# Optimization experiments

Hardware: AMD Instinct MI355X
Metric: run time of the kernel (lower is better)

## Reference

```python
import jax, jax.numpy as jnp
import numpy as np

B, NG, EG = 128, 256, 2048      # graphs, nodes/graph, edges/graph
N, E = B * NG, B * EG
D_NODE, D_EDGE, HID, HEADS = 64, 32, 128, 2
F1 = HEADS * HID                # 256
K = NG // 2                     # SAGPooling ratio=0.5 -> 128 nodes kept/graph


def _glorot(k, shape):
    fan_in = shape[0]
    return jax.random.normal(k, shape, jnp.float32) / np.sqrt(fan_in)


def setup_inputs() -> dict:
    key = jax.random.key(0)
    ks = jax.random.split(key, 26)
    x = jax.random.normal(ks[0], (N, D_NODE), jnp.float32)
    off = (jnp.arange(B, dtype=jnp.int32) * NG)[:, None]
    src = (jax.random.randint(ks[1], (B, EG), 0, NG, jnp.int32) + off).reshape(-1)
    dst = (jax.random.randint(ks[2], (B, EG), 0, NG, jnp.int32) + off).reshape(-1)
    edge_index = jnp.stack([src, dst])
    edge_attr = jax.random.normal(ks[3], (E, D_EDGE), jnp.float32)
    batch = jnp.repeat(jnp.arange(B, dtype=jnp.int32), NG)
    p = {
        'Wl1': _glorot(ks[4], (D_NODE, F1)), 'bl1': jnp.zeros((F1,), jnp.float32),
        'Wr1': _glorot(ks[5], (D_NODE, F1)), 'br1': jnp.zeros((F1,), jnp.float32),
        'We1': _glorot(ks[6], (D_EDGE, F1)),
        'att1': _glorot(ks[7], (HEADS, HID)), 'bout1': jnp.zeros((F1,), jnp.float32),
        'Wl2': _glorot(ks[8], (F1, F1)), 'bl2': jnp.zeros((F1,), jnp.float32),
        'Wr2': _glorot(ks[9], (F1, F1)), 'br2': jnp.zeros((F1,), jnp.float32),
        'We2': _glorot(ks[10], (D_EDGE, F1)),
        'att2': _glorot(ks[11], (1, F1)), 'bout2': jnp.zeros((F1,), jnp.float32),
        'Wrel': _glorot(ks[12], (F1, 1)), 'brel': jnp.zeros((1,), jnp.float32),
        'Wroot': _glorot(ks[13], (F1, 1)),
        'Wlin': _glorot(ks[14], (F1, 1)), 'blin': jnp.zeros((1,), jnp.float32),
    }
    return dict(x=x, edge_index=edge_index, edge_attr=edge_attr, batch=batch, **p)


def _gatv2(x, src, dst, eattr, Wl, bl, Wr, br, We, att, bout, heads, ch):
    n = x.shape[0]
    xl = (x @ Wl + bl).reshape(n, heads, ch)          # source transform (lin_l)
    xr = (x @ Wr + br).reshape(n, heads, ch)          # target transform (lin_r)
    ef = (eattr @ We).reshape(-1, heads, ch)
    m = xl[src] + xr[dst] + ef                        # [Etot, H, C]
    logits = jnp.einsum('ehc,hc->eh', jax.nn.leaky_relu(m, 0.2), att)
    mx = jax.lax.stop_gradient(jax.ops.segment_max(logits, dst, num_segments=n))
    ex = jnp.exp(logits - mx[dst])
    den = jax.ops.segment_sum(ex, dst, num_segments=n)
    alpha = ex / den[dst]                             # segment softmax per target
    out = jax.ops.segment_sum(alpha[:, :, None] * xl[src], dst, num_segments=n)
    return out.reshape(n, heads * ch) + bout


def reference(x, edge_index, edge_attr, batch,
              Wl1, bl1, Wr1, br1, We1, att1, bout1,
              Wl2, bl2, Wr2, br2, We2, att2, bout2,
              Wrel, brel, Wroot, Wlin, blin):
    n = x.shape[0]
    src, dst = edge_index[0], edge_index[1]
    # add_self_loops with fill_value='mean' of incoming edge attrs (PyG default)
    ones = jnp.ones((src.shape[0],), x.dtype)
    cnt = jax.ops.segment_sum(ones, dst, num_segments=n)
    loop_attr = jax.ops.segment_sum(edge_attr, dst, num_segments=n) / jnp.maximum(cnt, 1.0)[:, None]
    ar = jnp.arange(n, dtype=src.dtype)
    srcA = jnp.concatenate([src, ar])
    dstA = jnp.concatenate([dst, ar])
    eA = jnp.concatenate([edge_attr, loop_attr])
    # conv1: GATv2(64 -> 128, heads=2, concat)
    h = _gatv2(x, srcA, dstA, eA, Wl1, bl1, Wr1, br1, We1, att1, bout1, HEADS, HID)
    h = jax.nn.relu(h)
    # conv2: GATv2(256 -> 256, heads=1)
    h = _gatv2(h, srcA, dstA, eA, Wl2, bl2, Wr2, br2, We2, att2, bout2, 1, F1)
    # SAGPooling: GraphConv(256->1) scorer on original edges, tanh, top-k ratio=0.5
    agg = jax.ops.segment_sum(h[src], dst, num_segments=n)
    score = jnp.tanh((agg @ Wrel + brel + h @ Wroot).reshape(-1))
    sv, si = jax.lax.top_k(score.reshape(B, NG), K)   # equal-size graphs -> static k
    hg = h.reshape(B, NG, F1)
    xk = jnp.take_along_axis(hg, si[:, :, None], axis=1) * sv[:, :, None]
    xk = xk.reshape(B * K, F1)
    # dropout is identity in inference mode; final head
    return jax.nn.sigmoid(xk @ Wlin + blin)
```

## Files before the change

kernel.cpp:

```cpp
#include <hip/hip_runtime.h>
#include <math.h>

#define NNODES   32768
#define NEDGES   262144
#define EATOT    (NEDGES + NNODES)
#define NB       128
#define NGR      256
#define KKEEP    128
#define F1DIM    256
#define DNODE    64
#define DEDGE    32

__device__ __forceinline__ float xla_tanhf(float x) {
    float ax = fabsf(x);
    if (ax < 0.0004f) return x;
    if (ax > 7.90531110763549805f) return copysignf(1.0f, x);
    float x2 = __fmul_rn(x, x);
    float p = -2.76076847742355e-16f;
    p = fmaf(p, x2, 2.00018790482477e-13f);
    p = fmaf(p, x2, -8.60467152213735e-11f);
    p = fmaf(p, x2, 5.12229709037114e-08f);
    p = fmaf(p, x2, 1.48572235717979e-05f);
    p = fmaf(p, x2, 6.37261928875436e-04f);
    p = fmaf(p, x2, 4.89352455891786e-03f);
    p = __fmul_rn(x, p);
    float q = 1.19825839466702e-06f;
    q = fmaf(q, x2, 1.18534705686654e-04f);
    q = fmaf(q, x2, 2.26843463243900e-03f);
    q = fmaf(q, x2, 4.89352518554385e-03f);
    return __fdiv_rn(p, q);
}

__global__ void count_kernel(const int* __restrict__ ei, int* __restrict__ deg) {
    int t = blockIdx.x * 256 + threadIdx.x;
    if (t < NEDGES) atomicAdd(&deg[ei[NEDGES + t]], 1);
}

__global__ void scan_kernel(const int* __restrict__ deg, int* __restrict__ rowstart,
                            int* __restrict__ fill) {
    __shared__ int sh[1024];
    int t = threadIdx.x;
    int base = t * 32;
    int local[32];
    int s = 0;
#pragma unroll
    for (int i = 0; i < 32; i++) { local[i] = deg[base + i]; s += local[i]; }
    sh[t] = s;
    __syncthreads();
    for (int off = 1; off < 1024; off <<= 1) {
        int v = 0;
        if (t >= off) v = sh[t - off];
        __syncthreads();
        if (t >= off) sh[t] += v;
        __syncthreads();
    }
    int run = sh[t] - s;
#pragma unroll
    for (int i = 0; i < 32; i++) {
        rowstart[base + i] = run;
        fill[base + i] = run;
        run += local[i];
    }
    if (t == 1023) rowstart[NNODES] = run;
}

__global__ void scatter_kernel(const int* __restrict__ ei, int* __restrict__ fill,
                               int* __restrict__ csr) {
    int t = blockIdx.x * 256 + threadIdx.x;
    if (t < NEDGES) {
        int d = ei[NEDGES + t];
        int slot = atomicAdd(&fill[d], 1);
        csr[slot] = t;
    }
}

__global__ void sortcsr_kernel(const int* __restrict__ rowstart, int* __restrict__ csr) {
    int n = blockIdx.x * 256 + threadIdx.x;
    if (n >= NNODES) return;
    int s0 = rowstart[n], s1 = rowstart[n + 1];
    for (int i = s0 + 1; i < s1; i++) {
        int v = csr[i];
        int j = i - 1;
        while (j >= s0 && csr[j] > v) { csr[j + 1] = csr[j]; j--; }
        csr[j + 1] = v;
    }
}

__global__ void loopattr_kernel(const int* __restrict__ rowstart, const int* __restrict__ csr,
                                const float* __restrict__ eattr, float* __restrict__ loop_attr) {
    int t = blockIdx.x * 256 + threadIdx.x;
    int n = t >> 5, c = t & 31;
    int s0 = rowstart[n], s1 = rowstart[n + 1];
    float sum = 0.f;
    for (int i = s0; i < s1; i++) sum = __fadd_rn(sum, eattr[(size_t)csr[i] * DEDGE + c]);
    float cnt = (float)(s1 - s0);
    loop_attr[t] = __fdiv_rn(sum, fmaxf(cnt, 1.f));
}

template<int KD>
__global__ __launch_bounds__(256) void gemm_lr_kernel(
    const float* __restrict__ X,
    const float* __restrict__ Wl, const float* __restrict__ bl,
    const float* __restrict__ Wr, const float* __restrict__ br,
    float* __restrict__ outL, float* __restrict__ outR) {
    constexpr int NPB = 16;
    int n0 = __builtin_amdgcn_readfirstlane(blockIdx.x) * NPB;
    const float* __restrict__ Xb = X + (size_t)n0 * KD;
    int c = threadIdx.x;
    float accL[NPB], accR[NPB];
#pragma unroll
    for (int m = 0; m < NPB; m++) { accL[m] = 0.f; accR[m] = 0.f; }
    for (int k = 0; k < KD; k++) {
        float wl = Wl[k * F1DIM + c];
        float wr = Wr[k * F1DIM + c];
#pragma unroll
        for (int m = 0; m < NPB; m++) {
            float xv = Xb[m * KD + k];
            accL[m] = fmaf(xv, wl, accL[m]);
            accR[m] = fmaf(xv, wr, accR[m]);
        }
    }
    float blc = bl[c], brc = br[c];
#pragma unroll
    for (int m = 0; m < NPB; m++) {
        outL[(size_t)(n0 + m) * F1DIM + c] = __fadd_rn(accL[m], blc);
        outR[(size_t)(n0 + m) * F1DIM + c] = __fadd_rn(accR[m], brc);
    }
}

template<int H>
__global__ __launch_bounds__(256) void logits_kernel(
    const int* __restrict__ ei,
    const float* __restrict__ eattr, const float* __restrict__ loop_attr,
    const float* __restrict__ xl, const float* __restrict__ xr,
    const float* __restrict__ We, const float* __restrict__ att,
    float* __restrict__ logits) {
    constexpr int TILE = 8;
    constexpr int EPAD = 260;
    __shared__ float stageF[4][TILE * EPAD];
    int t = threadIdx.x;
    int lane = t & 63;
    int wv = t >> 6;

    float4 wreg[DEDGE];
#pragma unroll
    for (int k = 0; k < DEDGE; k++) wreg[k] = ((const float4*)We)[k * 64 + lane];
    float4 a4 = ((const float4*)att)[lane];

    int wid = (blockIdx.x * 256 + t) >> 6;
    int nw = (gridDim.x * 256) >> 6;
    int ntiles = EATOT / TILE;

    for (int tile = wid; tile < ntiles; tile += nw) {
        int ebase = __builtin_amdgcn_readfirstlane(tile) * TILE;

        for (int ee = 0; ee < TILE; ee++) {
            int e = ebase + ee;
            int s, d;
            const float* ea;
            if (e < NEDGES) {
                s = ei[e]; d = ei[NEDGES + e];
                ea = eattr + (size_t)e * DEDGE;
            } else {
                s = e - NEDGES; d = s;
                ea = loop_attr + (size_t)(e - NEDGES) * DEDGE;
            }
            s = __builtin_amdgcn_readfirstlane(s);
            d = __builtin_amdgcn_readfirstlane(d);
            float ef0 = 0.f, ef1 = 0.f, ef2 = 0.f, ef3 = 0.f;
#pragma unroll
            for (int k = 0; k < DEDGE; k++) {
                float eak = ea[k];
                ef0 = fmaf(eak, wreg[k].x, ef0);
                ef1 = fmaf(eak, wreg[k].y, ef1);
                ef2 = fmaf(eak, wreg[k].z, ef2);
                ef3 = fmaf(eak, wreg[k].w, ef3);
            }
            float4 l4 = ((const float4*)(xl + (size_t)s * F1DIM))[lane];
            float4 r4 = ((const float4*)(xr + (size_t)d * F1DIM))[lane];
            float mv, lk;
            float4 pv;
            mv = __fadd_rn(__fadd_rn(l4.x, r4.x), ef0);
            lk = mv > 0.f ? mv : __fmul_rn(0.2f, mv);
            pv.x = __fmul_rn(lk, a4.x);
            mv = __fadd_rn(__fadd_rn(l4.y, r4.y), ef1);
            lk = mv > 0.f ? mv : __fmul_rn(0.2f, mv);
            pv.y = __fmul_rn(lk, a4.y);
            mv = __fadd_rn(__fadd_rn(l4.z, r4.z), ef2);
            lk = mv > 0.f ? mv : __fmul_rn(0.2f, mv);
            pv.z = __fmul_rn(lk, a4.z);
            mv = __fadd_rn(__fadd_rn(l4.w, r4.w), ef3);
            lk = mv > 0.f ? mv : __fmul_rn(0.2f, mv);
            pv.w = __fmul_rn(lk, a4.w);
            *(float4*)&stageF[wv][ee * EPAD + lane * 4] = pv;
        }

        if (H == 2) {
            int edge = lane >> 3;
            int half = (lane >> 2) & 1;
            int j = lane & 3;
            const float* base = &stageF[wv][edge * EPAD + half * 128 + j];
            float s = 0.f;
#pragma unroll
            for (int L = 0; L < 32; L++)
                s = __fadd_rn(s, base[L * 4]);
            float o = __fadd_rn(s, __shfl_xor(s, 2));
            float r = __fadd_rn(o, __shfl_xor(o, 1));
            if (j == 0) logits[(size_t)(ebase + edge) * 2 + half] = r;
        } else {
            float s = 0.f;
            if (lane < 32) {
                int edge = lane >> 2;
                int j = lane & 3;
                const float* base = &stageF[wv][edge * EPAD + j];
#pragma unroll
                for (int L = 0; L < 64; L++)
                    s = __fadd_rn(s, base[L * 4]);
                float o = __fadd_rn(s, __shfl_xor(s, 2));
                float r = __fadd_rn(o, __shfl_xor(o, 1));
                if ((lane & 3) == 0) logits[ebase + (lane >> 2)] = r;
            }
        }
    }
}

template<int H>
__global__ void softmax_kernel(const int* __restrict__ rowstart, const int* __restrict__ csr,
                               const float* __restrict__ logits, float* __restrict__ w) {
    int t = blockIdx.x * 256 + threadIdx.x;
    if (t >= NNODES * H) return;
    int n = t / H;
    int h = t - n * H;
    int s0 = rowstart[n], s1 = rowstart[n + 1];
    float lself = logits[(size_t)(NEDGES + n) * H + h];
    float mx = lself;
    for (int i = s0; i < s1; i++) {
        float l = logits[(size_t)csr[i] * H + h];
        mx = fmaxf(mx, l);
    }
    float den = 0.f;
    for (int i = s0; i < s1; i++) {
        float ex = (float)exp((double)__fsub_rn(logits[(size_t)csr[i] * H + h], mx));
        den = __fadd_rn(den, ex);
    }
    float exs = (float)exp((double)__fsub_rn(lself, mx));
    den = __fadd_rn(den, exs);
    for (int i = s0; i < s1; i++) {
        size_t idx = (size_t)csr[i] * H + h;
        float ex = (float)exp((double)__fsub_rn(logits[idx], mx));
        w[idx] = __fdiv_rn(ex, den);
    }
    w[(size_t)(NEDGES + n) * H + h] = __fdiv_rn(exs, den);
}

template<int H, bool RELU>
__global__ __launch_bounds__(256) void agg_kernel(
    const int* __restrict__ ei, const int* __restrict__ rowstart, const int* __restrict__ csr,
    const float* __restrict__ w, const float* __restrict__ xl,
    const float* __restrict__ bout, float* __restrict__ out) {
    int n = blockIdx.x;
    int c = threadIdx.x;
    int h = (H == 2) ? (c >> 7) : 0;
    float acc = 0.f;
    int s0 = rowstart[n], s1 = rowstart[n + 1];
    for (int i = s0; i < s1; i++) {
        int e = csr[i];
        int sn = ei[e];
        float p = __fmul_rn(w[(size_t)e * H + h], xl[(size_t)sn * F1DIM + c]);
        acc = __fadd_rn(acc, p);
    }
    float pself = __fmul_rn(w[(size_t)(NEDGES + n) * H + h], xl[(size_t)n * F1DIM + c]);
    acc = __fadd_rn(acc, pself);
    acc = __fadd_rn(acc, bout[c]);
    if (RELU) acc = fmaxf(acc, 0.f);
    out[(size_t)n * F1DIM + c] = acc;
}

__global__ __launch_bounds__(256) void aggvec_kernel(
    const int* __restrict__ ei, const int* __restrict__ rowstart, const int* __restrict__ csr,
    const float* __restrict__ h2, float* __restrict__ aggv) {
    int n = blockIdx.x;
    int c = threadIdx.x;
    float acc = 0.f;
    int s0 = rowstart[n], s1 = rowstart[n + 1];
    for (int i = s0; i < s1; i++) {
        int sn = ei[csr[i]];
        acc = __fadd_rn(acc, h2[(size_t)sn * F1DIM + c]);
    }
    aggv[(size_t)n * F1DIM + c] = acc;
}

__global__ __launch_bounds__(256) void score_dots_kernel(
    const float* __restrict__ h2, const float* __restrict__ aggv,
    const float* __restrict__ Wrel, const float* __restrict__ Wroot,
    const float* __restrict__ brel, float* __restrict__ score) {
    __shared__ float wr[256], wo[256];
    int t = threadIdx.x;
    wr[t] = Wrel[t];
    wo[t] = Wroot[t];
    __syncthreads();
    int n = blockIdx.x * 256 + t;
    const float* hv = h2 + (size_t)n * F1DIM;
    const float* av = aggv + (size_t)n * F1DIM;
    float s1 = 0.f, s2 = 0.f;
    for (int c = 0; c < F1DIM; c++) {
        s1 = fmaf(av[c], wr[c], s1);
        s2 = fmaf(hv[c], wo[c], s2);
    }
    float u = __fadd_rn(__fadd_rn(s1, brel[0]), s2);
    score[n] = xla_tanhf(u);
}

__global__ __launch_bounds__(256) void topk_kernel(
    const float* __restrict__ score, const float* __restrict__ h2,
    const float* __restrict__ Wlin, const float* __restrict__ blin,
    float* __restrict__ out) {
    __shared__ float sv[256];
    __shared__ int si[256];
    __shared__ float wl[256];
    int t = threadIdx.x;
    int g = blockIdx.x;
    sv[t] = score[g * NGR + t];
    si[t] = t;
    wl[t] = Wlin[t];
    __syncthreads();
    for (int k = 2; k <= 256; k <<= 1) {
        for (int j = k >> 1; j > 0; j >>= 1) {
            int ixj = t ^ j;
            if (ixj > t) {
                float va = sv[t], vb = sv[ixj];
                int ia = si[t], ib = si[ixj];
                bool before = (va > vb) || (va == vb && ia < ib);
                bool up = ((t & k) == 0);
                if (up ? !before : before) {
                    sv[t] = vb; sv[ixj] = va;
                    si[t] = ib; si[ixj] = ia;
                }
            }
            __syncthreads();
        }
    }
    if (t < KKEEP) {
        float v = sv[t];
        int idx = si[t];
        const float* hv = h2 + (size_t)(g * NGR + idx) * F1DIM;
        float acc = 0.f;
        for (int c = 0; c < F1DIM; c++) {
            float xc = __fmul_rn(hv[c], v);
            acc = fmaf(xc, wl[c], acc);
        }
        float z = __fadd_rn(acc, blin[0]);
        out[g * KKEEP + t] = (float)(1.0 / (1.0 + exp(-(double)z)));
    }
}

extern "C" void kernel_launch(void* const* d_in, const int* in_sizes, int n_in,
                              void* d_out, int out_size, void* d_ws, size_t ws_size,
                              hipStream_t stream) {
    const float* x        = (const float*)d_in[0];
    const int*   ei       = (const int*)d_in[1];
    const float* eattr    = (const float*)d_in[2];
    const float* Wl1  = (const float*)d_in[4];
    const float* bl1  = (const float*)d_in[5];
    const float* Wr1  = (const float*)d_in[6];
    const float* br1  = (const float*)d_in[7];
    const float* We1  = (const float*)d_in[8];
    const float* att1 = (const float*)d_in[9];
    const float* bout1= (const float*)d_in[10];
    const float* Wl2  = (const float*)d_in[11];
    const float* bl2  = (const float*)d_in[12];
    const float* Wr2  = (const float*)d_in[13];
    const float* br2  = (const float*)d_in[14];
    const float* We2  = (const float*)d_in[15];
    const float* att2 = (const float*)d_in[16];
    const float* bout2= (const float*)d_in[17];
    const float* Wrel = (const float*)d_in[18];
    const float* brel = (const float*)d_in[19];
    const float* Wroot= (const float*)d_in[20];
    const float* Wlin = (const float*)d_in[21];
    const float* blin = (const float*)d_in[22];
    float* out = (float*)d_out;

    char* p = (char*)d_ws;
    auto alloc = [&](size_t bytes) {
        void* r = (void*)p;
        p += (bytes + 255) & ~(size_t)255;
        return r;
    };
    int*   deg      = (int*)alloc(NNODES * 4);
    int*   rowstart = (int*)alloc((NNODES + 1) * 4);
    int*   fill     = (int*)alloc(NNODES * 4);
    int*   csr      = (int*)alloc(NEDGES * 4);
    float* loop_attr= (float*)alloc((size_t)NNODES * DEDGE * 4);
    float* bufA     = (float*)alloc((size_t)NNODES * F1DIM * 4);
    float* bufB     = (float*)alloc((size_t)NNODES * F1DIM * 4);
    float* bufC     = (float*)alloc((size_t)NNODES * F1DIM * 4);
    float* logitsB  = (float*)alloc((size_t)EATOT * 2 * 4);
    float* wB       = (float*)alloc((size_t)EATOT * 2 * 4);
    float* scoreV   = (float*)alloc(NNODES * 4);

    hipMemsetAsync(deg, 0, NNODES * 4, stream);
    count_kernel<<<NEDGES / 256, 256, 0, stream>>>(ei, deg);
    scan_kernel<<<1, 1024, 0, stream>>>(deg, rowstart, fill);
    scatter_kernel<<<NEDGES / 256, 256, 0, stream>>>(ei, fill, csr);
    sortcsr_kernel<<<NNODES / 256, 256, 0, stream>>>(rowstart, csr);
    loopattr_kernel<<<NNODES * DEDGE / 256, 256, 0, stream>>>(rowstart, csr, eattr, loop_attr);

    gemm_lr_kernel<DNODE><<<NNODES / 16, 256, 0, stream>>>(x, Wl1, bl1, Wr1, br1, bufA, bufB);
    logits_kernel<2><<<2048, 256, 0, stream>>>(ei, eattr, loop_attr, bufA, bufB, We1, att1, logitsB);
    softmax_kernel<2><<<(NNODES * 2) / 256, 256, 0, stream>>>(rowstart, csr, logitsB, wB);
    agg_kernel<2, true><<<NNODES, 256, 0, stream>>>(ei, rowstart, csr, wB, bufA, bout1, bufC);

    gemm_lr_kernel<F1DIM><<<NNODES / 16, 256, 0, stream>>>(bufC, Wl2, bl2, Wr2, br2, bufA, bufB);
    logits_kernel<1><<<2048, 256, 0, stream>>>(ei, eattr, loop_attr, bufA, bufB, We2, att2, logitsB);
    softmax_kernel<1><<<NNODES / 256, 256, 0, stream>>>(rowstart, csr, logitsB, wB);
    agg_kernel<1, false><<<NNODES, 256, 0, stream>>>(ei, rowstart, csr, wB, bufA, bout2, bufC);

    aggvec_kernel<<<NNODES, 256, 0, stream>>>(ei, rowstart, csr, bufC, bufA);
    score_dots_kernel<<<NNODES / 256, 256, 0, stream>>>(bufC, bufA, Wrel, Wroot, brel, scoreV);
    topk_kernel<<<NB, 256, 0, stream>>>(scoreV, bufC, Wlin, blin, out);
}
```

Before: 865.4 us.

## Register-tile GEMM with LDS-staged X and float4 weight loads

Restructures the node-transform GEMM so each block handles 64 nodes: X tiles are staged transposed in shared memory and each thread computes a 16x4 register tile for both left and right outputs using float4 weight loads. This raises arithmetic intensity and cuts redundant global weight and X reads compared with the old 16-node, one-column-per-thread scheme. The 128 accumulators per thread raise register pressure and may lower occupancy, and the grid shrinks by four times.

After: 895.0 us. 1.03x slower.

```diff
diff --git a/kernel.cpp b/kernel.cpp
--- a/kernel.cpp
+++ b/kernel.cpp
@@ -103,28 +103,68 @@
     const float* __restrict__ Wl, const float* __restrict__ bl,
     const float* __restrict__ Wr, const float* __restrict__ br,
     float* __restrict__ outL, float* __restrict__ outR) {
-    constexpr int NPB = 16;
-    int n0 = __builtin_amdgcn_readfirstlane(blockIdx.x) * NPB;
-    const float* __restrict__ Xb = X + (size_t)n0 * KD;
-    int c = threadIdx.x;
-    float accL[NPB], accR[NPB];
-#pragma unroll
-    for (int m = 0; m < NPB; m++) { accL[m] = 0.f; accR[m] = 0.f; }
-    for (int k = 0; k < KD; k++) {
-        float wl = Wl[k * F1DIM + c];
-        float wr = Wr[k * F1DIM + c];
-#pragma unroll
-        for (int m = 0; m < NPB; m++) {
-            float xv = Xb[m * KD + k];
-            accL[m] = fmaf(xv, wl, accL[m]);
-            accR[m] = fmaf(xv, wr, accR[m]);
-        }
-    }
-    float blc = bl[c], brc = br[c];
-#pragma unroll
-    for (int m = 0; m < NPB; m++) {
-        outL[(size_t)(n0 + m) * F1DIM + c] = __fadd_rn(accL[m], blc);
-        outR[(size_t)(n0 + m) * F1DIM + c] = __fadd_rn(accR[m], brc);
+    constexpr int NN = 64;
+    constexpr int KC = 64;
+    constexpr int P  = 68;
+    __shared__ float xs[KC * P];
+    int t = threadIdx.x;
+    int lane = t & 63;
+    int g = t >> 6;
+    int n0 = blockIdx.x * NN;
+
+    float accL[16][4], accR[16][4];
+#pragma unroll
+    for (int m = 0; m < 16; m++)
+#pragma unroll
+        for (int j = 0; j < 4; j++) { accL[m][j] = 0.f; accR[m][j] = 0.f; }
+
+    for (int k0 = 0; k0 < KD; k0 += KC) {
+        __syncthreads();
+        for (int i = t; i < NN * KC; i += 256) {
+            int m = i >> 6;
+            int kk = i & 63;
+            xs[kk * P + m] = X[(size_t)(n0 + m) * KD + k0 + kk];
+        }
+        __syncthreads();
+        for (int kk = 0; kk < KC; kk++) {
+            float4 wl4 = ((const float4*)(Wl + (size_t)(k0 + kk) * F1DIM))[lane];
+            float4 wr4 = ((const float4*)(Wr + (size_t)(k0 + kk) * F1DIM))[lane];
+            const float* xb = &xs[kk * P + g * 16];
+            float xv[16];
+            *(float4*)&xv[0]  = *(const float4*)(xb + 0);
+            *(float4*)&xv[4]  = *(const float4*)(xb + 4);
+            *(float4*)&xv[8]  = *(const float4*)(xb + 8);
+            *(float4*)&xv[12] = *(const float4*)(xb + 12);
+#pragma unroll
+            for (int m = 0; m < 16; m++) {
+                accL[m][0] = fmaf(xv[m], wl4.x, accL[m][0]);
+                accL[m][1] = fmaf(xv[m], wl4.y, accL[m][1]);
+                accL[m][2] = fmaf(xv[m], wl4.z, accL[m][2]);
+                accL[m][3] = fmaf(xv[m], wl4.w, accL[m][3]);
+                accR[m][0] = fmaf(xv[m], wr4.x, accR[m][0]);
+                accR[m][1] = fmaf(xv[m], wr4.y, accR[m][1]);
+                accR[m][2] = fmaf(xv[m], wr4.z, accR[m][2]);
+                accR[m][3] = fmaf(xv[m], wr4.w, accR[m][3]);
+            }
+        }
+    }
+
+    float4 bl4 = ((const float4*)bl)[lane];
+    float4 br4 = ((const float4*)br)[lane];
+#pragma unroll
+    for (int m = 0; m < 16; m++) {
+        int n = n0 + g * 16 + m;
+        float4 oL, oR;
+        oL.x = __fadd_rn(accL[m][0], bl4.x);
+        oL.y = __fadd_rn(accL[m][1], bl4.y);
+        oL.z = __fadd_rn(accL[m][2], bl4.z);
+        oL.w = __fadd_rn(accL[m][3], bl4.w);
+        oR.x = __fadd_rn(accR[m][0], br4.x);
+        oR.y = __fadd_rn(accR[m][1], br4.y);
+        oR.z = __fadd_rn(accR[m][2], br4.z);
+        oR.w = __fadd_rn(accR[m][3], br4.w);
+        ((float4*)(outL + (size_t)n * F1DIM))[lane] = oL;
+        ((float4*)(outR + (size_t)n * F1DIM))[lane] = oR;
     }
 }
 
@@ -406,12 +446,12 @@
     sortcsr_kernel<<<NNODES / 256, 256, 0, stream>>>(rowstart, csr);
     loopattr_kernel<<<NNODES * DEDGE / 256, 256, 0, stream>>>(rowstart, csr, eattr, loop_attr);
 
-    gemm_lr_kernel<DNODE><<<NNODES / 16, 256, 0, stream>>>(x, Wl1, bl1, Wr1, br1, bufA, bufB);
+    gemm_lr_kernel<DNODE><<<NNODES / 64, 256, 0, stream>>>(x, Wl1, bl1, Wr1, br1, bufA, bufB);
     logits_kernel<2><<<2048, 256, 0, stream>>>(ei, eattr, loop_attr, bufA, bufB, We1, att1, logitsB);
     softmax_kernel<2><<<(NNODES * 2) / 256, 256, 0, stream>>>(rowstart, csr, logitsB, wB);
     agg_kernel<2, true><<<NNODES, 256, 0, stream>>>(ei, rowstart, csr, wB, bufA, bout1, bufC);
 
-    gemm_lr_kernel<F1DIM><<<NNODES / 16, 256, 0, stream>>>(bufC, Wl2, bl2, Wr2, br2, bufA, bufB);
+    gemm_lr_kernel<F1DIM><<<NNODES / 64, 256, 0, stream>>>(bufC, Wl2, bl2, Wr2, br2, bufA, bufB);
     logits_kernel<1><<<2048, 256, 0, stream>>>(ei, eattr, loop_attr, bufA, bufB, We2, att2, logitsB);
     softmax_kernel<1><<<NNODES / 256, 256, 0, stream>>>(rowstart, csr, logitsB, wB);
     agg_kernel<1, false><<<NNODES, 256, 0, stream>>>(ei, rowstart, csr, wB, bufA, bout2, bufC);
```
